# Kernel tuning notes

Measured on AMD Instinct MI355X. Metric: run time of the kernel, lower is better.

## Reference

```python
import jax, jax.numpy as jnp
import numpy as np

B, N, D = 1, 4096, 3072
H, DH = 16, 64
INNER = H * DH  # 1024
SCALE = DH ** -0.5
EPS = 1e-5


def setup_inputs() -> dict:
    key = jax.random.key(0)
    ks = jax.random.split(key, 4)
    x = jax.random.normal(ks[0], (B, N, D), jnp.float32)
    pe = jax.random.normal(ks[1], (1, 1, N, DH // 2, 2, 2), jnp.float32)
    w_qkv = jax.random.normal(ks[2], (3 * INNER, D), jnp.float32) * 0.02
    w_out = jax.random.normal(ks[3], (D, INNER), jnp.float32) * 0.02
    ln_g = jnp.ones((D,), jnp.float32)
    ln_b = jnp.zeros((D,), jnp.float32)
    return {"x": x, "pe": pe, "w_qkv": w_qkv, "w_out": w_out, "ln_g": ln_g, "ln_b": ln_b}


def _apply_rope(t, pe):
    # t: [b,h,n,d], pe: [1,1,n,d/2,2,2] (Flux rope layout)
    b, h, n, d = t.shape
    t_ = t.reshape(b, h, n, d // 2, 1, 2)
    out = pe[..., 0] * t_[..., 0] + pe[..., 1] * t_[..., 1]  # [b,h,n,d/2,2]
    return out.reshape(b, h, n, d)


def reference(x, pe, w_qkv, w_out, ln_g, ln_b):
    # LayerNorm (norm2)
    mu = jnp.mean(x, axis=-1, keepdims=True)
    var = jnp.mean((x - mu) ** 2, axis=-1, keepdims=True)
    xn = (x - mu) / jnp.sqrt(var + EPS) * ln_g + ln_b
    # QKV projection (no bias)
    qkv = xn @ w_qkv.T  # [b,n,3*inner]
    q, k, v = jnp.split(qkv, 3, axis=-1)
    def split_heads(t):
        return t.reshape(B, N, H, DH).transpose(0, 2, 1, 3)  # b h n d
    q, k, v = split_heads(q), split_heads(k), split_heads(v)
    # RoPE on q and k (attention_aug_bbox with mask=None, aug idx = -1 -> plain rope attn)
    q = _apply_rope(q, pe)
    k = _apply_rope(k, pe)
    scores = jnp.einsum('bhqd,bhkd->bhqk', q, k) * SCALE
    attn = jax.nn.softmax(scores, axis=-1)
    o = jnp.einsum('bhqk,bhkd->bhqd', attn, v)
    o = o.transpose(0, 2, 1, 3).reshape(B, N, INNER)  # b n (h d)
    return o @ w_out.T  # [b,n,dim]
```

## Files before the change

### kernel.cpp

```cpp
#include <hip/hip_runtime.h>
#include <hip/hip_bf16.h>

typedef unsigned short u16;
typedef __attribute__((ext_vector_type(8))) short bf16x8;
typedef __attribute__((ext_vector_type(4))) float f32x4;

#define N_TOK 4096
#define DMODEL 3072
#define NH 16
#define DHEAD 64
#define INNER 1024
#define SCALE_LOG2E 0.18033688011112042f

__device__ __forceinline__ u16 f2bf(float f) {
    union { float f; unsigned u; } un; un.f = f;
    unsigned r = un.u + 0x7fffu + ((un.u >> 16) & 1u);
    return (u16)(r >> 16);
}
__device__ __forceinline__ float bf2f(u16 u) {
    union { unsigned u; float f; } x; x.u = ((unsigned)u) << 16; return x.f;
}
__device__ __forceinline__ unsigned pk2bf(float a, float b) {
    union { float f; unsigned u; } ua, ub; ua.f = a; ub.f = b;
    return __builtin_amdgcn_perm(ub.u + 0x8000u, ua.u + 0x8000u, 0x07060302u);
}
__device__ __forceinline__ void load_lds16(const u16* g, u16* l) {
    __builtin_amdgcn_global_load_lds(
        (const __attribute__((address_space(1))) unsigned int*)g,
        (__attribute__((address_space(3))) unsigned int*)l, 16, 0, 0);
}

__device__ __forceinline__ bf16x8 build_bp(unsigned u0, unsigned u1,
                                           unsigned w0, unsigned w1) {
    auto a = __builtin_amdgcn_permlane32_swap(u0, w0, false, false);
    auto b = __builtin_amdgcn_permlane16_swap(a[0], a[1], false, false);
    auto c = __builtin_amdgcn_permlane32_swap(u1, w1, false, false);
    auto d = __builtin_amdgcn_permlane16_swap(c[0], c[1], false, false);
    union { unsigned w[4]; bf16x8 v; } r;
    r.w[0] = b[0]; r.w[1] = d[0]; r.w[2] = b[1]; r.w[3] = d[1];
    return r.v;
}

__global__ __launch_bounds__(256) void prep(const float* __restrict__ x,
                                            const float* __restrict__ g,
                                            const float* __restrict__ b,
                                            u16* __restrict__ xn,
                                            const float* __restrict__ w_qkv,
                                            u16* __restrict__ wq,
                                            const float* __restrict__ w_out,
                                            u16* __restrict__ wo) {
    int bid = blockIdx.x;
    int tid = threadIdx.x;
    if (bid < 4096) {
        int row = bid;
        const float4* xr = (const float4*)(x + (size_t)row * DMODEL);
        float4 v[3];
        float s = 0.f, ss = 0.f;
#pragma unroll
        for (int i = 0; i < 3; ++i) {
            v[i] = xr[i * 256 + tid];
            s  += v[i].x + v[i].y + v[i].z + v[i].w;
            ss += v[i].x * v[i].x + v[i].y * v[i].y + v[i].z * v[i].z + v[i].w * v[i].w;
        }
#pragma unroll
        for (int off = 32; off; off >>= 1) {
            s  += __shfl_xor(s, off);
            ss += __shfl_xor(ss, off);
        }
        __shared__ float red[8];
        int wid = tid >> 6, lane = tid & 63;
        if (lane == 0) { red[wid] = s; red[wid + 4] = ss; }
        __syncthreads();
        s  = red[0] + red[1] + red[2] + red[3];
        ss = red[4] + red[5] + red[6] + red[7];
        float mean = s * (1.f / DMODEL);
        float var  = ss * (1.f / DMODEL) - mean * mean;
        float rstd = rsqrtf(var + 1e-5f);
        ushort4* orow = (ushort4*)(xn + (size_t)row * DMODEL);
#pragma unroll
        for (int i = 0; i < 3; ++i) {
            float4 gg = ((const float4*)g)[i * 256 + tid];
            float4 bb = ((const float4*)b)[i * 256 + tid];
            ushort4 o;
            o.x = f2bf((v[i].x - mean) * rstd * gg.x + bb.x);
            o.y = f2bf((v[i].y - mean) * rstd * gg.y + bb.y);
            o.z = f2bf((v[i].z - mean) * rstd * gg.z + bb.z);
            o.w = f2bf((v[i].w - mean) * rstd * gg.w + bb.w);
            orow[i * 256 + tid] = o;
        }
    } else if (bid < 4096 + 2048) {
        const int n4 = 3 * INNER * DMODEL / 4;
        for (int i = (bid - 4096) * 256 + tid; i < n4; i += 2048 * 256) {
            float4 v = ((const float4*)w_qkv)[i];
            ushort4 o;
            o.x = f2bf(v.x); o.y = f2bf(v.y); o.z = f2bf(v.z); o.w = f2bf(v.w);
            ((ushort4*)wq)[i] = o;
        }
    } else {
        const int n4 = DMODEL * INNER / 4;
        for (int i = (bid - 6144) * 256 + tid; i < n4; i += 512 * 256) {
            float4 v = ((const float4*)w_out)[i];
            ushort4 o;
            o.x = f2bf(v.x); o.y = f2bf(v.y); o.z = f2bf(v.z); o.w = f2bf(v.w);
            ((ushort4*)wo)[i] = o;
        }
    }
}


#define VM6 asm volatile("s_waitcnt vmcnt(6)" ::: "memory")
#define VM4 asm volatile("s_waitcnt vmcnt(4)" ::: "memory")
#define VM0 asm volatile("s_waitcnt vmcnt(0)" ::: "memory")
#define LGK8 asm volatile("s_waitcnt lgkmcnt(8)" ::: "memory")
#define NOPS ((void)0)

#define ST_A(d, h, t) do { \
    load_lds16(pA##h##0 + (size_t)(t) * 64, &lds[(d) * 16384 + (h) * 8192 + dq]); \
    load_lds16(pA##h##1 + (size_t)(t) * 64, &lds[(d) * 16384 + (h) * 8192 + dq + 512]); \
  } while (0)
#define ST_B(d, h, t) do { \
    load_lds16(pB##h##0 + (size_t)(t) * 64, &lds[32768 + (d) * 16384 + (h) * 8192 + dq]); \
    load_lds16(pB##h##1 + (size_t)(t) * 64, &lds[32768 + (d) * 16384 + (h) * 8192 + dq + 512]); \
  } while (0)

#define PHASE(d, p, STAGE, PRE, POST) do { \
    bf16x8 afr[2][2]; \
    if ((p) == 0) { \
      _Pragma("unroll") for (int nf = 0; nf < 4; ++nf) { \
        bfr[nf][0] = *(const bf16x8*)&lds[(d) * 16384 + baseB + nf * 1024 + c0]; \
        bfr[nf][1] = *(const bf16x8*)&lds[(d) * 16384 + baseB + nf * 1024 + c1]; \
      } \
    } \
    _Pragma("unroll") for (int mfl = 0; mfl < 2; ++mfl) { \
      afr[mfl][0] = *(const bf16x8*)&lds[(d) * 16384 + (p) * 4096 + mfl * 1024 + baseA + c0]; \
      afr[mfl][1] = *(const bf16x8*)&lds[(d) * 16384 + (p) * 4096 + mfl * 1024 + baseA + c1]; \
    } \
    STAGE; \
    PRE; \
    __builtin_amdgcn_s_barrier(); \
    asm volatile("s_waitcnt lgkmcnt(0)" ::: "memory"); \
    __builtin_amdgcn_sched_barrier(0); \
    __builtin_amdgcn_s_setprio(1); \
    _Pragma("unroll") for (int mfl = 0; mfl < 2; ++mfl) \
      _Pragma("unroll") for (int nf = 0; nf < 4; ++nf) { \
        acc[(p) * 2 + mfl][nf] = __builtin_amdgcn_mfma_f32_16x16x32_bf16(afr[mfl][0], bfr[nf][0], acc[(p) * 2 + mfl][nf], 0, 0, 0); \
        acc[(p) * 2 + mfl][nf] = __builtin_amdgcn_mfma_f32_16x16x32_bf16(afr[mfl][1], bfr[nf][1], acc[(p) * 2 + mfl][nf], 0, 0, 0); \
      } \
    __builtin_amdgcn_s_setprio(0); \
    POST; \
    __builtin_amdgcn_s_barrier(); \
  } while (0)

template <int MODE>
__global__ __launch_bounds__(512, 2) void gemm256(const u16* __restrict__ A,
                                                  const u16* __restrict__ B,
                                                  void* __restrict__ C,
                                                  int M, int Nn, int K,
                                                  const float* __restrict__ pe,
                                                  u16* __restrict__ Qr,
                                                  u16* __restrict__ Kr,
                                                  u16* __restrict__ Vt) {
    __shared__ u16 lds[65536];
    const int tid = threadIdx.x;
    const int lane = tid & 63, wid = tid >> 6;
    const int wm = wid >> 2, wn = wid & 3;
    const int l15 = lane & 15, quad = lane >> 4;
    const int sw = l15 & 7;

    int nbx = Nn >> 8;
    int cpx = gridDim.x >> 3;
    int wg = (blockIdx.x & 7) * cpx + (blockIdx.x >> 3);
    int m0 = (wg / nbx) << 8, n0 = (wg % nbx) << 8;

    const int baseA = wm * 2048 + l15 * 64;
    const int baseB = 32768 + wn * 4096 + l15 * 64;
    const int c0 = (quad ^ sw) * 8;
    const int c1 = ((4 + quad) ^ sw) * 8;
    const int dq = wid * 1024;

    const u16 *pA00, *pA01, *pA10, *pA11, *pB00, *pB01, *pB10, *pB11;
    {
        int scol = ((lane & 7) ^ (lane >> 3)) * 8;
#define MKSRC(h, j, PA, PB) { \
        int ell = (h) * 128 + (wid * 2 + (j)) * 8 + (lane >> 3); \
        int g = ell >> 6, wmh = (ell >> 5) & 1, r = ell & 31; \
        PA = A + (size_t)(m0 + wmh * 128 + g * 32 + r) * K + scol; \
        PB = B + (size_t)(n0 + ell) * K + scol; }
        MKSRC(0, 0, pA00, pB00) MKSRC(0, 1, pA01, pB01)
        MKSRC(1, 0, pA10, pB10) MKSRC(1, 1, pA11, pB11)
#undef MKSRC
    }

    f32x4 acc[8][4];
    f32x4 zero4 = {0.f, 0.f, 0.f, 0.f};
#pragma unroll
    for (int i = 0; i < 8; ++i)
#pragma unroll
        for (int j = 0; j < 4; ++j) acc[i][j] = zero4;
    bf16x8 bfr[4][2];

    ST_B(0, 0, 0); ST_B(0, 1, 0); ST_A(0, 0, 0); ST_A(0, 1, 0);
    ST_B(1, 0, 1); ST_B(1, 1, 1); ST_A(1, 0, 1);
    VM6;
    __builtin_amdgcn_s_barrier();

    const int NIT = (K >> 7) - 1;
    for (int i = 0; i < NIT; ++i) {
        int t = 2 * i;
        PHASE(0, 0, ST_A(1, 1, t + 1), LGK8, NOPS);
        PHASE(0, 1, ST_B(0, 0, t + 2), NOPS, NOPS);
        PHASE(0, 2, ST_B(0, 1, t + 2), NOPS, NOPS);
        PHASE(0, 3, ST_A(0, 0, t + 2), NOPS, VM6);
        PHASE(1, 0, ST_A(0, 1, t + 2), LGK8, NOPS);
        PHASE(1, 1, ST_B(1, 0, t + 3), NOPS, NOPS);
        PHASE(1, 2, ST_B(1, 1, t + 3), NOPS, NOPS);
        PHASE(1, 3, ST_A(1, 0, t + 3), NOPS, VM6);
    }
    {
        int T = K >> 6;
        PHASE(0, 0, ST_A(1, 1, T - 1), LGK8, NOPS);
        PHASE(0, 1, NOPS, NOPS, NOPS);
        PHASE(0, 2, NOPS, NOPS, NOPS);
        PHASE(0, 3, NOPS, NOPS, VM0);
        PHASE(1, 0, NOPS, LGK8, NOPS);
        PHASE(1, 1, NOPS, NOPS, NOPS);
        PHASE(1, 2, NOPS, NOPS, NOPS);
        PHASE(1, 3, NOPS, NOPS, NOPS);
    }

    if (MODE == 0) {
#pragma unroll
        for (int mf = 0; mf < 8; ++mf)
#pragma unroll
            for (int nf = 0; nf < 4; ++nf)
#pragma unroll
                for (int r = 0; r < 4; ++r) {
                    int rr = m0 + wm * 128 + mf * 16 + quad * 4 + r;
                    int cc = n0 + wn * 64 + nf * 16 + l15;
                    ((float*)C)[(size_t)rr * Nn + cc] = acc[mf][nf][r];
                }
    } else if (n0 < 2048) {
        const int isQ = (n0 < 1024);
        const float scl = isQ ? SCALE_LOG2E : 1.f;
        u16* dst = isQ ? Qr : Kr;
#pragma unroll
        for (int mf = 0; mf < 8; ++mf)
#pragma unroll
            for (int nf = 0; nf < 4; ++nf) {
                int cc = n0 + wn * 64 + nf * 16 + l15;
                int hh = (cc & 1023) >> 6;
                int ii = (cc & 63) >> 1;
                int jj = cc & 1;
#pragma unroll
                for (int r = 0; r < 4; ++r) {
                    int rr = m0 + wm * 128 + mf * 16 + quad * 4 + r;
                    float v = acc[mf][nf][r];
                    float vp = __shfl_xor(v, 1);
                    float v0 = jj ? vp : v;
                    float v1 = jj ? v : vp;
                    const float* pw = pe + (size_t)rr * 128 + ii * 4 + jj * 2;
                    float ov = (pw[0] * v0 + pw[1] * v1) * scl;
                    dst[((size_t)hh * N_TOK + rr) * 64 + (cc & 63)] = f2bf(ov);
                }
            }
    } else {
#pragma unroll
        for (int mf = 0; mf < 8; ++mf)
#pragma unroll
            for (int nf = 0; nf < 4; ++nf) {
                int cc = n0 + wn * 64 + nf * 16 + l15;
                int hh = (cc - 2048) >> 6, dd = cc & 63;
                int rr = m0 + wm * 128 + mf * 16 + quad * 4;
                ushort4 o4;
                o4.x = f2bf(acc[mf][nf][0]); o4.y = f2bf(acc[mf][nf][1]);
                o4.z = f2bf(acc[mf][nf][2]); o4.w = f2bf(acc[mf][nf][3]);
                *(ushort4*)&Vt[((size_t)hh * 64 + dd) * N_TOK + rr] = o4;
            }
    }
}


#define FA_STAGE3(dst, kt) do { \
    load_lds16(&Kh[(size_t)((kt) + krow) * DHEAD + csw], &lds_all[(dst) + kbase]); \
    load_lds16(&Kh[(size_t)((kt) + krow + 8) * DHEAD + csw], &lds_all[(dst) + kbase + 512]); \
    load_lds16(&Vh[(size_t)krow * N_TOK + (kt) + csw], &lds_all[(dst) + 4096 + kbase]); \
    load_lds16(&Vh[(size_t)(krow + 8) * N_TOK + (kt) + csw], &lds_all[(dst) + 4096 + kbase + 512]); \
  } while (0)

__global__ __launch_bounds__(256, 2) void flash_attn(const u16* __restrict__ Q,
                                                     const u16* __restrict__ K,
                                                     const u16* __restrict__ Vt,
                                                     u16* __restrict__ O) {
    __shared__ u16 lds_all[24576];
    int tid = threadIdx.x, lane = tid & 63, wid = tid >> 6;
    int l15 = lane & 15, quad = lane >> 4;
    int sw = l15 & 7;
    int h = blockIdx.y;
    int q0 = blockIdx.x * 128 + wid * 32;
    const u16* Qh = Q + (size_t)h * N_TOK * DHEAD;
    const u16* Kh = K + (size_t)h * N_TOK * DHEAD;
    const u16* Vh = Vt + (size_t)h * DHEAD * N_TOK;

    f32x4 zero4 = {0.f, 0.f, 0.f, 0.f};
    bf16x8 ones;
#pragma unroll
    for (int i = 0; i < 8; ++i) ones[i] = (short)0x3F80;

    bf16x8 aq[2][2];
#pragma unroll
    for (int mtQ = 0; mtQ < 2; ++mtQ)
#pragma unroll
        for (int kc = 0; kc < 2; ++kc)
            aq[mtQ][kc] = *(const bf16x8*)&Qh[(size_t)(q0 + mtQ * 16 + l15) * DHEAD + kc * 32 + quad * 8];

    f32x4 o[2][4], lacc[2];
#pragma unroll
    for (int mtQ = 0; mtQ < 2; ++mtQ) {
#pragma unroll
        for (int dt = 0; dt < 4; ++dt) o[mtQ][dt] = zero4;
        lacc[mtQ] = zero4;
    }

    int rowoff = lane >> 3;
    int krow = wid * 16 + rowoff;
    int kbase = wid * 1024;
    int csw = ((lane & 7) ^ rowoff) * 8;

    FA_STAGE3(0, 0);
    FA_STAGE3(8192, 64);
    VM4;
    __builtin_amdgcn_s_barrier();
    __builtin_amdgcn_sched_barrier(0);

    int cur = 0;
    for (int t = 0; t < 64; ++t) {
        int stg = cur + 16384; if (stg >= 24576) stg -= 24576;
        bf16x8 bk[4][2], av[4][2];
#pragma unroll
        for (int tt = 0; tt < 4; ++tt)
#pragma unroll
            for (int kc = 0; kc < 2; ++kc)
                bk[tt][kc] = *(const bf16x8*)&lds_all[cur + (tt * 16 + l15) * 64 + (((kc * 4 + quad) ^ sw) * 8)];
        __builtin_amdgcn_sched_barrier(0);
#pragma unroll
        for (int tt = 0; tt < 4; ++tt)
#pragma unroll
            for (int kc = 0; kc < 2; ++kc)
                av[tt][kc] = *(const bf16x8*)&lds_all[cur + 4096 + (tt * 16 + l15) * 64 + (((kc * 4 + quad) ^ sw) * 8)];
        __builtin_amdgcn_sched_barrier(0);
        if (t < 62) FA_STAGE3(stg, (t + 2) * 64);
        asm volatile("s_waitcnt lgkmcnt(8)" ::: "memory");
        __builtin_amdgcn_sched_barrier(0);

        bf16x8 bp[2][2];
#pragma unroll
        for (int mtQ = 0; mtQ < 2; ++mtQ) {
            f32x4 s[4];
            __builtin_amdgcn_s_setprio(1);
#pragma unroll
            for (int ntK = 0; ntK < 4; ++ntK) {
                f32x4 t0 = __builtin_amdgcn_mfma_f32_16x16x32_bf16(bk[ntK][0], aq[mtQ][0], zero4, 0, 0, 0);
                s[ntK] = __builtin_amdgcn_mfma_f32_16x16x32_bf16(bk[ntK][1], aq[mtQ][1], t0, 0, 0, 0);
            }
            __builtin_amdgcn_s_setprio(0);
            unsigned pw[4][2];
#pragma unroll
            for (int ntK = 0; ntK < 4; ++ntK) {
                pw[ntK][0] = pk2bf(__builtin_amdgcn_exp2f(s[ntK][0]), __builtin_amdgcn_exp2f(s[ntK][1]));
                pw[ntK][1] = pk2bf(__builtin_amdgcn_exp2f(s[ntK][2]), __builtin_amdgcn_exp2f(s[ntK][3]));
            }
            bp[mtQ][0] = build_bp(pw[0][0], pw[0][1], pw[1][0], pw[1][1]);
            bp[mtQ][1] = build_bp(pw[2][0], pw[2][1], pw[3][0], pw[3][1]);
        }

        asm volatile("s_waitcnt lgkmcnt(0)" ::: "memory");
        __builtin_amdgcn_sched_barrier(0);
        __builtin_amdgcn_s_setprio(1);
#pragma unroll
        for (int mtQ = 0; mtQ < 2; ++mtQ) {
            lacc[mtQ] = __builtin_amdgcn_mfma_f32_16x16x32_bf16(ones, bp[mtQ][0], lacc[mtQ], 0, 0, 0);
            lacc[mtQ] = __builtin_amdgcn_mfma_f32_16x16x32_bf16(ones, bp[mtQ][1], lacc[mtQ], 0, 0, 0);
#pragma unroll
            for (int dt = 0; dt < 4; ++dt) {
                o[mtQ][dt] = __builtin_amdgcn_mfma_f32_16x16x32_bf16(av[dt][0], bp[mtQ][0], o[mtQ][dt], 0, 0, 0);
                o[mtQ][dt] = __builtin_amdgcn_mfma_f32_16x16x32_bf16(av[dt][1], bp[mtQ][1], o[mtQ][dt], 0, 0, 0);
            }
        }
        __builtin_amdgcn_s_setprio(0);

        if (t < 62) { VM4; } else if (t == 62) { VM0; }
        __builtin_amdgcn_s_barrier();
        __builtin_amdgcn_sched_barrier(0);
        cur += 8192; if (cur >= 24576) cur -= 24576;
    }

    __syncthreads();
    u16* scratch = lds_all + wid * 2048;
#pragma unroll
    for (int mtQ = 0; mtQ < 2; ++mtQ) {
        float rl = 1.f / lacc[mtQ][0];
#pragma unroll
        for (int dt = 0; dt < 4; ++dt) {
            uint2 ov;
            ov.x = pk2bf(o[mtQ][dt][0] * rl, o[mtQ][dt][1] * rl);
            ov.y = pk2bf(o[mtQ][dt][2] * rl, o[mtQ][dt][3] * rl);
            *(uint2*)&scratch[(mtQ * 16 + l15) * 64 + dt * 16 + quad * 4] = ov;
        }
    }
    __syncthreads();
#pragma unroll
    for (int p = 0; p < 4; ++p) {
        int q_local = p * 8 + (lane >> 3);
        int dcol = (lane & 7) * 8;
        bf16x8 v = *(const bf16x8*)&scratch[q_local * 64 + dcol];
        *(bf16x8*)&O[(size_t)(q0 + q_local) * INNER + h * 64 + dcol] = v;
    }
}

extern "C" void kernel_launch(void* const* d_in, const int* in_sizes, int n_in,
                              void* d_out, int out_size, void* d_ws, size_t ws_size,
                              hipStream_t stream) {
    const float* x     = (const float*)d_in[0];
    const float* pe    = (const float*)d_in[1];
    const float* w_qkv = (const float*)d_in[2];
    const float* w_out = (const float*)d_in[3];
    const float* ln_g  = (const float*)d_in[4];
    const float* ln_b  = (const float*)d_in[5];
    float* out = (float*)d_out;

    char* ws = (char*)d_ws;
    u16* xn  = (u16*)ws;  ws += (size_t)N_TOK * DMODEL * 2;
    u16* wq  = (u16*)ws;  ws += (size_t)3 * INNER * DMODEL * 2;
    u16* wo  = (u16*)ws;  ws += (size_t)DMODEL * INNER * 2;
    u16* Qr  = (u16*)ws;  ws += (size_t)NH * N_TOK * DHEAD * 2;
    u16* Kr  = (u16*)ws;  ws += (size_t)NH * N_TOK * DHEAD * 2;
    u16* Vt  = (u16*)ws;  ws += (size_t)NH * DHEAD * N_TOK * 2;
    u16* Ob  = (u16*)ws;  ws += (size_t)N_TOK * INNER * 2;

    prep<<<4096 + 2048 + 512, 256, 0, stream>>>(x, ln_g, ln_b, xn, w_qkv, wq, w_out, wo);
    gemm256<2><<<dim3((N_TOK / 256) * (DMODEL / 256)), 512, 0, stream>>>(
        xn, wq, nullptr, N_TOK, DMODEL, DMODEL, pe, Qr, Kr, Vt);
    flash_attn<<<dim3(N_TOK / 128, NH), 256, 0, stream>>>(Qr, Kr, Vt, Ob);
    gemm256<0><<<dim3((N_TOK / 256) * (DMODEL / 256)), 512, 0, stream>>>(
        Ob, wo, out, N_TOK, DMODEL, INNER, nullptr, nullptr, nullptr, nullptr);
}
```

Baseline: 357.3 us.

## Use 256x192 GEMM tiles so the grid fills all compute units

Changes the GEMM block tile from 256x256 to 256x192, giving 256 workgroups instead of 192 for both projections. The B staging is split into three 64-row chunks, the pipeline wait counts are retuned, and the QKV epilogue now decides per column between Q/K RoPE and V output. The intent is to remove the wave-quantization idle time of the 192-block grid. In exchange, each tile does less arithmetic per loaded A byte and the staging schedule is less balanced.

```diff
diff --git a/kernel.cpp b/kernel.cpp
--- a/kernel.cpp
+++ b/kernel.cpp
@@ -108,8 +108,9 @@
 }
 
 
-#define VM6 asm volatile("s_waitcnt vmcnt(6)" ::: "memory")
+#define VM5 asm volatile("s_waitcnt vmcnt(5)" ::: "memory")
 #define VM4 asm volatile("s_waitcnt vmcnt(4)" ::: "memory")
+#define VM3 asm volatile("s_waitcnt vmcnt(3)" ::: "memory")
 #define VM0 asm volatile("s_waitcnt vmcnt(0)" ::: "memory")
 #define LGK8 asm volatile("s_waitcnt lgkmcnt(8)" ::: "memory")
 #define NOPS ((void)0)
@@ -118,17 +119,15 @@
     load_lds16(pA##h##0 + (size_t)(t) * 64, &lds[(d) * 16384 + (h) * 8192 + dq]); \
     load_lds16(pA##h##1 + (size_t)(t) * 64, &lds[(d) * 16384 + (h) * 8192 + dq + 512]); \
   } while (0)
-#define ST_B(d, h, t) do { \
-    load_lds16(pB##h##0 + (size_t)(t) * 64, &lds[32768 + (d) * 16384 + (h) * 8192 + dq]); \
-    load_lds16(pB##h##1 + (size_t)(t) * 64, &lds[32768 + (d) * 16384 + (h) * 8192 + dq + 512]); \
-  } while (0)
+#define ST_B1(d, u, t) \
+    load_lds16(pB##u + (size_t)(t) * 64, &lds[32768 + (d) * 12288 + (u) * 4096 + wid * 512])
 
 #define PHASE(d, p, STAGE, PRE, POST) do { \
     bf16x8 afr[2][2]; \
     if ((p) == 0) { \
-      _Pragma("unroll") for (int nf = 0; nf < 4; ++nf) { \
-        bfr[nf][0] = *(const bf16x8*)&lds[(d) * 16384 + baseB + nf * 1024 + c0]; \
-        bfr[nf][1] = *(const bf16x8*)&lds[(d) * 16384 + baseB + nf * 1024 + c1]; \
+      _Pragma("unroll") for (int nf = 0; nf < 3; ++nf) { \
+        bfr[nf][0] = *(const bf16x8*)&lds[32768 + (d) * 12288 + baseB + nf * 1024 + c0]; \
+        bfr[nf][1] = *(const bf16x8*)&lds[32768 + (d) * 12288 + baseB + nf * 1024 + c1]; \
       } \
     } \
     _Pragma("unroll") for (int mfl = 0; mfl < 2; ++mfl) { \
@@ -142,7 +141,7 @@
     __builtin_amdgcn_sched_barrier(0); \
     __builtin_amdgcn_s_setprio(1); \
     _Pragma("unroll") for (int mfl = 0; mfl < 2; ++mfl) \
-      _Pragma("unroll") for (int nf = 0; nf < 4; ++nf) { \
+      _Pragma("unroll") for (int nf = 0; nf < 3; ++nf) { \
         acc[(p) * 2 + mfl][nf] = __builtin_amdgcn_mfma_f32_16x16x32_bf16(afr[mfl][0], bfr[nf][0], acc[(p) * 2 + mfl][nf], 0, 0, 0); \
         acc[(p) * 2 + mfl][nf] = __builtin_amdgcn_mfma_f32_16x16x32_bf16(afr[mfl][1], bfr[nf][1], acc[(p) * 2 + mfl][nf], 0, 0, 0); \
       } \
@@ -160,61 +159,65 @@
                                                   u16* __restrict__ Qr,
                                                   u16* __restrict__ Kr,
                                                   u16* __restrict__ Vt) {
-    __shared__ u16 lds[65536];
+    __shared__ u16 lds[57344];
     const int tid = threadIdx.x;
     const int lane = tid & 63, wid = tid >> 6;
     const int wm = wid >> 2, wn = wid & 3;
     const int l15 = lane & 15, quad = lane >> 4;
     const int sw = l15 & 7;
 
-    int nbx = Nn >> 8;
+    int nbx = Nn / 192;
     int cpx = gridDim.x >> 3;
     int wg = (blockIdx.x & 7) * cpx + (blockIdx.x >> 3);
-    int m0 = (wg / nbx) << 8, n0 = (wg % nbx) << 8;
+    int m0 = (wg / nbx) << 8, n0 = (wg % nbx) * 192;
 
     const int baseA = wm * 2048 + l15 * 64;
-    const int baseB = 32768 + wn * 4096 + l15 * 64;
+    const int baseB = wn * 3072 + l15 * 64;
     const int c0 = (quad ^ sw) * 8;
     const int c1 = ((4 + quad) ^ sw) * 8;
     const int dq = wid * 1024;
 
-    const u16 *pA00, *pA01, *pA10, *pA11, *pB00, *pB01, *pB10, *pB11;
+    const u16 *pA00, *pA01, *pA10, *pA11, *pB0, *pB1, *pB2;
     {
         int scol = ((lane & 7) ^ (lane >> 3)) * 8;
-#define MKSRC(h, j, PA, PB) { \
+#define MKSRCA(h, j, PA) { \
         int ell = (h) * 128 + (wid * 2 + (j)) * 8 + (lane >> 3); \
         int g = ell >> 6, wmh = (ell >> 5) & 1, r = ell & 31; \
-        PA = A + (size_t)(m0 + wmh * 128 + g * 32 + r) * K + scol; \
+        PA = A + (size_t)(m0 + wmh * 128 + g * 32 + r) * K + scol; }
+#define MKSRCB(u, PB) { \
+        int ell = (u) * 64 + wid * 8 + (lane >> 3); \
         PB = B + (size_t)(n0 + ell) * K + scol; }
-        MKSRC(0, 0, pA00, pB00) MKSRC(0, 1, pA01, pB01)
-        MKSRC(1, 0, pA10, pB10) MKSRC(1, 1, pA11, pB11)
-#undef MKSRC
-    }
-
-    f32x4 acc[8][4];
+        MKSRCA(0, 0, pA00) MKSRCA(0, 1, pA01)
+        MKSRCA(1, 0, pA10) MKSRCA(1, 1, pA11)
+        MKSRCB(0, pB0) MKSRCB(1, pB1) MKSRCB(2, pB2)
+#undef MKSRCA
+#undef MKSRCB
+    }
+
+    f32x4 acc[8][3];
     f32x4 zero4 = {0.f, 0.f, 0.f, 0.f};
 #pragma unroll
     for (int i = 0; i < 8; ++i)
 #pragma unroll
-        for (int j = 0; j < 4; ++j) acc[i][j] = zero4;
-    bf16x8 bfr[4][2];
-
-    ST_B(0, 0, 0); ST_B(0, 1, 0); ST_A(0, 0, 0); ST_A(0, 1, 0);
-    ST_B(1, 0, 1); ST_B(1, 1, 1); ST_A(1, 0, 1);
-    VM6;
+        for (int j = 0; j < 3; ++j) acc[i][j] = zero4;
+    bf16x8 bfr[3][2];
+
+    ST_B1(0, 0, 0); ST_B1(0, 1, 0); ST_B1(0, 2, 0); ST_A(0, 0, 0); ST_A(0, 1, 0);
+    ST_B1(1, 0, 1); ST_B1(1, 1, 1); ST_B1(1, 2, 1); ST_A(1, 0, 1);
+    VM5;
     __builtin_amdgcn_s_barrier();
 
     const int NIT = (K >> 7) - 1;
     for (int i = 0; i < NIT; ++i) {
         int t = 2 * i;
         PHASE(0, 0, ST_A(1, 1, t + 1), LGK8, NOPS);
-        PHASE(0, 1, ST_B(0, 0, t + 2), NOPS, NOPS);
-        PHASE(0, 2, ST_B(0, 1, t + 2), NOPS, NOPS);
-        PHASE(0, 3, ST_A(0, 0, t + 2), NOPS, VM6);
-        PHASE(1, 0, ST_A(0, 1, t + 2), LGK8, NOPS);
-        PHASE(1, 1, ST_B(1, 0, t + 3), NOPS, NOPS);
-        PHASE(1, 2, ST_B(1, 1, t + 3), NOPS, NOPS);
-        PHASE(1, 3, ST_A(1, 0, t + 3), NOPS, VM6);
+        PHASE(0, 1, ST_B1(0, 0, t + 2), NOPS, NOPS);
+        PHASE(0, 2, ST_B1(0, 1, t + 2), NOPS, NOPS);
+        PHASE(0, 3, ST_B1(0, 2, t + 2), NOPS, VM3);
+        PHASE(1, 0, ST_A(0, 0, t + 2), LGK8, NOPS);
+        PHASE(1, 1, ST_A(0, 1, t + 2), NOPS, NOPS);
+        PHASE(1, 2, ST_B1(1, 0, t + 3), NOPS, NOPS);
+        PHASE(1, 3, { ST_B1(1, 1, t + 3); ST_B1(1, 2, t + 3); ST_A(1, 0, t + 3); }, NOPS, VM5);
     }
     {
         int T = K >> 6;
@@ -232,50 +235,49 @@
 #pragma unroll
         for (int mf = 0; mf < 8; ++mf)
 #pragma unroll
-            for (int nf = 0; nf < 4; ++nf)
+            for (int nf = 0; nf < 3; ++nf)
 #pragma unroll
                 for (int r = 0; r < 4; ++r) {
                     int rr = m0 + wm * 128 + mf * 16 + quad * 4 + r;
-                    int cc = n0 + wn * 64 + nf * 16 + l15;
+                    int cc = n0 + wn * 48 + nf * 16 + l15;
                     ((float*)C)[(size_t)rr * Nn + cc] = acc[mf][nf][r];
                 }
-    } else if (n0 < 2048) {
-        const int isQ = (n0 < 1024);
-        const float scl = isQ ? SCALE_LOG2E : 1.f;
-        u16* dst = isQ ? Qr : Kr;
-#pragma unroll
-        for (int mf = 0; mf < 8; ++mf)
-#pragma unroll
-            for (int nf = 0; nf < 4; ++nf) {
-                int cc = n0 + wn * 64 + nf * 16 + l15;
+    } else {
+#pragma unroll
+        for (int nf = 0; nf < 3; ++nf) {
+            int cc = n0 + wn * 48 + nf * 16 + l15;
+            if (cc < 2048) {
+                const int isQ = (cc < 1024);
+                const float scl = isQ ? SCALE_LOG2E : 1.f;
+                u16* dst = isQ ? Qr : Kr;
                 int hh = (cc & 1023) >> 6;
                 int ii = (cc & 63) >> 1;
                 int jj = cc & 1;
 #pragma unroll
-                for (int r = 0; r < 4; ++r) {
-                    int rr = m0 + wm * 128 + mf * 16 + quad * 4 + r;
-                    float v = acc[mf][nf][r];
-                    float vp = __shfl_xor(v, 1);
-                    float v0 = jj ? vp : v;
-                    float v1 = jj ? v : vp;
-                    const float* pw = pe + (size_t)rr * 128 + ii * 4 + jj * 2;
-                    float ov = (pw[0] * v0 + pw[1] * v1) * scl;
-                    dst[((size_t)hh * N_TOK + rr) * 64 + (cc & 63)] = f2bf(ov);
+                for (int mf = 0; mf < 8; ++mf)
+#pragma unroll
+                    for (int r = 0; r < 4; ++r) {
+                        int rr = m0 + wm * 128 + mf * 16 + quad * 4 + r;
+                        float v = acc[mf][nf][r];
+                        float vp = __shfl_xor(v, 1);
+                        float v0 = jj ? vp : v;
+                        float v1 = jj ? v : vp;
+                        const float* pw = pe + (size_t)rr * 128 + ii * 4 + jj * 2;
+                        float ov = (pw[0] * v0 + pw[1] * v1) * scl;
+                        dst[((size_t)hh * N_TOK + rr) * 64 + (cc & 63)] = f2bf(ov);
+                    }
+            } else {
+                int hh = (cc - 2048) >> 6, dd = cc & 63;
+#pragma unroll
+                for (int mf = 0; mf < 8; ++mf) {
+                    int rr = m0 + wm * 128 + mf * 16 + quad * 4;
+                    ushort4 o4;
+                    o4.x = f2bf(acc[mf][nf][0]); o4.y = f2bf(acc[mf][nf][1]);
+                    o4.z = f2bf(acc[mf][nf][2]); o4.w = f2bf(acc[mf][nf][3]);
+                    *(ushort4*)&Vt[((size_t)hh * 64 + dd) * N_TOK + rr] = o4;
                 }
             }
-    } else {
-#pragma unroll
-        for (int mf = 0; mf < 8; ++mf)
-#pragma unroll
-            for (int nf = 0; nf < 4; ++nf) {
-                int cc = n0 + wn * 64 + nf * 16 + l15;
-                int hh = (cc - 2048) >> 6, dd = cc & 63;
-                int rr = m0 + wm * 128 + mf * 16 + quad * 4;
-                ushort4 o4;
-                o4.x = f2bf(acc[mf][nf][0]); o4.y = f2bf(acc[mf][nf][1]);
-                o4.z = f2bf(acc[mf][nf][2]); o4.w = f2bf(acc[mf][nf][3]);
-                *(ushort4*)&Vt[((size_t)hh * 64 + dd) * N_TOK + rr] = o4;
-            }
+        }
     }
 }
 
@@ -438,9 +440,9 @@
     u16* Ob  = (u16*)ws;  ws += (size_t)N_TOK * INNER * 2;
 
     prep<<<4096 + 2048 + 512, 256, 0, stream>>>(x, ln_g, ln_b, xn, w_qkv, wq, w_out, wo);
-    gemm256<2><<<dim3((N_TOK / 256) * (DMODEL / 256)), 512, 0, stream>>>(
+    gemm256<2><<<dim3((N_TOK / 256) * (DMODEL / 192)), 512, 0, stream>>>(
         xn, wq, nullptr, N_TOK, DMODEL, DMODEL, pe, Qr, Kr, Vt);
     flash_attn<<<dim3(N_TOK / 128, NH), 256, 0, stream>>>(Qr, Kr, Vt, Ob);
-    gemm256<0><<<dim3((N_TOK / 256) * (DMODEL / 256)), 512, 0, stream>>>(
+    gemm256<0><<<dim3((N_TOK / 256) * (DMODEL / 192)), 512, 0, stream>>>(
         Ob, wo, out, N_TOK, DMODEL, INNER, nullptr, nullptr, nullptr, nullptr);
 }
```

After: 348.9 us. -2.3%, faster.
